# Performance work log

Hardware: AMD Instinct MI355X
Metric: run time of the kernel (lower is better)

## Reference

```python
import jax, jax.numpy as jnp
import numpy as np

B, S, D, H = 4, 2048, 1024, 16
DH = D // H


def setup_inputs() -> dict:
    key = jax.random.key(0)
    ks = jax.random.split(key, 11)
    s = 1.0 / np.sqrt(D)
    return {
        "q": jax.random.normal(ks[0], (B, S, D), jnp.float32),
        "k": jax.random.normal(ks[1], (B, S, D), jnp.float32),
        "v": jax.random.normal(ks[2], (B, S, D), jnp.float32),
        "Wq": jax.random.normal(ks[3], (D, D), jnp.float32) * s,
        "bq": jnp.zeros((D,), jnp.float32),
        "Wk": jax.random.normal(ks[4], (D, D), jnp.float32) * s,
        "bk": jnp.zeros((D,), jnp.float32),
        "Wv": jax.random.normal(ks[5], (D, D), jnp.float32) * s,
        "bv": jnp.zeros((D,), jnp.float32),
        "Wo": jax.random.normal(ks[6], (D, D), jnp.float32) * s,
        "bo": jnp.zeros((D,), jnp.float32),
    }


def _split_heads(x):
    # (B, S, D) -> (B, H, S, DH)
    b, s, _ = x.shape
    return x.reshape(b, s, H, DH).transpose(0, 2, 1, 3)


def reference(q, k, v, Wq, bq, Wk, bk, Wv, bv, Wo, bo):
    # torch Linear: x @ W.T + b
    qh = _split_heads(q @ Wq.T + bq)
    kh = _split_heads(k @ Wk.T + bk)
    vh = _split_heads(v @ Wv.T + bv)
    scale = 1.0 / jnp.sqrt(jnp.asarray(DH, qh.dtype))
    scores = jnp.einsum("bhqd,bhkd->bhqk", qh, kh) * scale  # (B,H,S,S)
    probs = jax.nn.softmax(scores, axis=-1)
    ctx = jnp.einsum("bhqk,bhkd->bhqd", probs, vh)  # (B,H,S,DH)
    x = ctx.transpose(0, 2, 1, 3).reshape(q.shape[0], -1, D)
    return x @ Wo.T + bo
```

## Files before the change

kernel.cpp:

```cpp
#include <hip/hip_runtime.h>

typedef __bf16 bf16x8 __attribute__((ext_vector_type(8)));
typedef __bf16 bf16x4 __attribute__((ext_vector_type(4)));
typedef _Float16 f16x8 __attribute__((ext_vector_type(8)));
typedef _Float16 f16x4v __attribute__((ext_vector_type(4)));
typedef __fp16 fp16x2 __attribute__((ext_vector_type(2)));
typedef float f32x4 __attribute__((ext_vector_type(4)));
typedef float f32x16 __attribute__((ext_vector_type(16)));
typedef unsigned short u16;
typedef unsigned int u32;
typedef unsigned int u32x4 __attribute__((ext_vector_type(4)));

constexpr int Bc = 4, Sc = 2048, Dc = 1024, Hc = 16, DHc = 64;
constexpr int Mrows = Bc * Sc;
constexpr size_t MK = (size_t)Mrows * Dc;
constexpr size_t WK = (size_t)Dc * Dc;

__device__ __forceinline__ u16 f2bf(float f) {
  u32 u = __float_as_uint(f);
  u = (u + 0x7fffu + ((u >> 16) & 1u)) >> 16;
  return (u16)u;
}

#define LDSP(p) ((__attribute__((address_space(3))) void*)(p))
#define GLBP(p) ((const __attribute__((address_space(1))) void*)(p))

__global__ __launch_bounds__(256) void cvt4_kernel(const float* __restrict__ a,
                                                   const float* __restrict__ b,
                                                   const float* __restrict__ c,
                                                   const float* __restrict__ d,
                                                   ushort4* __restrict__ out, int n4) {
  const float4* in = (const float4*)(blockIdx.y == 0 ? a : blockIdx.y == 1 ? b
                                     : blockIdx.y == 2 ? c : d);
  ushort4* o = out + (size_t)blockIdx.y * n4;
  int stride = gridDim.x * blockDim.x;
  for (int i = blockIdx.x * blockDim.x + threadIdx.x; i < n4; i += stride) {
    float4 v = in[i];
    ushort4 r;
    r.x = f2bf(v.x); r.y = f2bf(v.y); r.z = f2bf(v.z); r.w = f2bf(v.w);
    o[i] = r;
  }
}

__global__ __launch_bounds__(256, 2) void gemmqkv(const float* __restrict__ Aq,
                                                  const float* __restrict__ Ak,
                                                  const float* __restrict__ Av,
                                                  const u16* __restrict__ Bt0,
                                                  const float* __restrict__ b0,
                                                  const float* __restrict__ b1,
                                                  const float* __restrict__ b2,
                                                  void* __restrict__ out0) {
  constexpr int K = 1024, NT = 32;
  __shared__ u16 lds[3 * 12288];

  const int y = blockIdx.y;
  const float* A = (y == 0) ? Aq : (y == 1) ? Ak : Av;
  const u16* Bt = Bt0 + (size_t)y * WK;
  const float* bias = (y == 0) ? b0 : (y == 1) ? b1 : b2;

  const int wg = (blockIdx.x & 7) * 32 + (blockIdx.x >> 3);
  const int tm = wg >> 3, tn = wg & 7;
  const int row0 = tm << 8, col0 = tn << 7;

  const int t_ = threadIdx.x, w = t_ >> 6, l = t_ & 63;
  const int wm = w >> 1, wn = w & 1;
  const int col = l & 31, hh = l >> 5;

  f32x16 acc[4][2] = {};
  float4 areg[8];

  auto ldA = [&](int tile) {
#pragma unroll
    for (int i = 0; i < 4; ++i) {
      const int r = (w * 4 + i) * 16 + (l >> 2);
      const float* p = A + (size_t)(row0 + r) * K + (tile << 5) + (l & 3) * 8;
      areg[2 * i] = *(const float4*)p;
      areg[2 * i + 1] = *(const float4*)(p + 4);
    }
  };
  auto wrA = [&](int tile) {
    u16* buf = &lds[(tile % 3) * 12288];
#pragma unroll
    for (int i = 0; i < 4; ++i) {
      const int r = (w * 4 + i) * 16 + (l >> 2);
      u32 d0, d1, d2, d3;
      asm("v_cvt_pk_bf16_f32 %0, %1, %2" : "=v"(d0) : "v"(areg[2 * i].x), "v"(areg[2 * i].y));
      asm("v_cvt_pk_bf16_f32 %0, %1, %2" : "=v"(d1) : "v"(areg[2 * i].z), "v"(areg[2 * i].w));
      asm("v_cvt_pk_bf16_f32 %0, %1, %2" : "=v"(d2) : "v"(areg[2 * i + 1].x), "v"(areg[2 * i + 1].y));
      asm("v_cvt_pk_bf16_f32 %0, %1, %2" : "=v"(d3) : "v"(areg[2 * i + 1].z), "v"(areg[2 * i + 1].w));
      u32x4 pk; pk[0] = d0; pk[1] = d1; pk[2] = d2; pk[3] = d3;
      const int g = (l & 3) ^ ((r >> 1) & 3);
      *(u32x4*)((char*)buf + r * 64 + g * 16) = pk;
    }
  };
  auto stB = [&](int tile, int i) {
    u16* buf = &lds[(tile % 3) * 12288] + 8192;
    const int c = w * 2 + i;
    const int r = c * 16 + (l >> 2);
    const int sg = (l & 3) ^ ((r >> 1) & 3);
    __builtin_amdgcn_global_load_lds(
        GLBP(Bt + (size_t)(col0 + r) * K + (tile << 5) + sg * 8),
        LDSP(buf + c * 512), 16, 0, 0);
  };

  ldA(0);
  stB(0, 0); stB(0, 1);
  stB(1, 0); stB(1, 1);
  asm volatile("s_waitcnt vmcnt(2)" ::: "memory");
  wrA(0);
  ldA(1);
  asm volatile("s_waitcnt lgkmcnt(0)" ::: "memory");
  __builtin_amdgcn_s_barrier();

#pragma unroll 1
  for (int t = 0; t < NT; ++t) {
    const u16* abuf = &lds[(t % 3) * 12288];
    const u16* bbuf = abuf + 8192;
    if (t + 2 < NT) { stB(t + 2, 0); stB(t + 2, 1); }
    bf16x8 af[2][4], bf[2][2];
#pragma unroll
    for (int kc = 0; kc < 2; ++kc) {
      const int g = kc * 2 + hh;
#pragma unroll
      for (int mb = 0; mb < 4; ++mb) {
        const int ar = wm * 128 + mb * 32 + col;
        af[kc][mb] = *(const bf16x8*)&abuf[ar * 32 + ((g ^ ((ar >> 1) & 3)) << 3)];
      }
#pragma unroll
      for (int nb = 0; nb < 2; ++nb) {
        const int br = wn * 64 + nb * 32 + col;
        bf[kc][nb] = *(const bf16x8*)&bbuf[br * 32 + ((g ^ ((br >> 1) & 3)) << 3)];
      }
    }
    __builtin_amdgcn_s_setprio(1);
#pragma unroll
    for (int kc = 0; kc < 2; ++kc)
#pragma unroll
      for (int mb = 0; mb < 4; ++mb)
#pragma unroll
        for (int nb = 0; nb < 2; ++nb)
          acc[mb][nb] = __builtin_amdgcn_mfma_f32_32x32x16_bf16(af[kc][mb], bf[kc][nb],
                                                               acc[mb][nb], 0, 0, 0);
    __builtin_amdgcn_s_setprio(0);
    if (t + 1 < NT) {
      if (t + 2 < NT) asm volatile("s_waitcnt vmcnt(2)" ::: "memory");
      else            asm volatile("s_waitcnt vmcnt(0)" ::: "memory");
      wrA(t + 1);
      if (t + 2 < NT) ldA(t + 2);
    }
    asm volatile("s_waitcnt lgkmcnt(0)" ::: "memory");
    __builtin_amdgcn_s_barrier();
  }

#pragma unroll
  for (int mb = 0; mb < 4; ++mb)
#pragma unroll
    for (int nb = 0; nb < 2; ++nb) {
      const int n = col0 + wn * 64 + nb * 32 + col;
      const float bv = bias[n];
      const int mbase = row0 + wm * 128 + mb * 32 + 4 * hh;
      if (y == 2) {
        u16* Vt = (u16*)out0 + 2 * MK;
        const int h = n >> 6, dh = n & 63;
#pragma unroll
        for (int qg = 0; qg < 4; ++qg) {
          const int s0 = mbase + 8 * qg;
          const int b = s0 >> 11, s = s0 & (Sc - 1);
          f16x4v pk;
#pragma unroll
          for (int r4 = 0; r4 < 4; ++r4) pk[r4] = (_Float16)(acc[mb][nb][qg * 4 + r4] + bv);
          *(f16x4v*)&Vt[((size_t)((b * Hc + h) * DHc + dh)) * Sc + s] = pk;
        }
      } else {
        u16* Oh = (u16*)out0 + (size_t)y * MK;
        const float scl = (y == 0) ? 0.125f * 1.44269504089f : 1.f;
        const int h = n >> 6, dh = n & 63;
#pragma unroll
        for (int r = 0; r < 16; ++r) {
          const int m = mbase + (r & 3) + 8 * (r >> 2);
          const int b = m >> 11, s = m & (Sc - 1);
          Oh[((size_t)((b * Hc + h) * Sc + s)) * DHc + dh] = f2bf((acc[mb][nb][r] + bv) * scl);
        }
      }
    }
}

__global__ __launch_bounds__(256, 2) void gemmout(const u16* __restrict__ A,
                                                  const u16* __restrict__ Bt,
                                                  const float* __restrict__ bias,
                                                  float* __restrict__ O) {
  constexpr int K = 1024, NT = 32;
  __shared__ u16 lds[3 * 12288];

  const int wg = (blockIdx.x & 7) * 32 + (blockIdx.x >> 3);
  const int tm = wg >> 3, tn = wg & 7;
  const int row0 = tm << 8, col0 = tn << 7;

  const int t_ = threadIdx.x, w = t_ >> 6, l = t_ & 63;
  const int wm = w >> 1, wn = w & 1;
  const int col = l & 31, hh = l >> 5;

  f32x16 acc[4][2] = {};

  auto stA = [&](int tile, int i) {
    u16* buf = &lds[(tile % 3) * 12288];
    const int c = w * 4 + i;
    const int r = c * 16 + (l >> 2);
    const int sg = (l & 3) ^ ((r >> 1) & 3);
    __builtin_amdgcn_global_load_lds(
        GLBP(A + (size_t)(row0 + r) * K + (tile << 5) + sg * 8),
        LDSP(buf + c * 512), 16, 0, 0);
  };
  auto stB = [&](int tile, int i) {
    u16* buf = &lds[(tile % 3) * 12288] + 8192;
    const int c = w * 2 + i;
    const int r = c * 16 + (l >> 2);
    const int sg = (l & 3) ^ ((r >> 1) & 3);
    __builtin_amdgcn_global_load_lds(
        GLBP(Bt + (size_t)(col0 + r) * K + (tile << 5) + sg * 8),
        LDSP(buf + c * 512), 16, 0, 0);
  };

  stA(0, 0); stA(0, 1); stA(0, 2); stA(0, 3); stB(0, 0); stB(0, 1);
  stA(1, 0); stA(1, 1); stA(1, 2); stA(1, 3); stB(1, 0); stB(1, 1);
  asm volatile("s_waitcnt vmcnt(6)" ::: "memory");
  __builtin_amdgcn_s_barrier();

#pragma unroll 1
  for (int t = 0; t < NT; ++t) {
    const u16* abuf = &lds[(t % 3) * 12288];
    const u16* bbuf = abuf + 8192;
    if (t + 2 < NT) {
      stA(t + 2, 0); stA(t + 2, 1); stA(t + 2, 2); stA(t + 2, 3);
      stB(t + 2, 0); stB(t + 2, 1);
    }
    bf16x8 af[2][4], bf[2][2];
#pragma unroll
    for (int kc = 0; kc < 2; ++kc) {
      const int g = kc * 2 + hh;
#pragma unroll
      for (int mb = 0; mb < 4; ++mb) {
        const int ar = wm * 128 + mb * 32 + col;
        af[kc][mb] = *(const bf16x8*)&abuf[ar * 32 + ((g ^ ((ar >> 1) & 3)) << 3)];
      }
#pragma unroll
      for (int nb = 0; nb < 2; ++nb) {
        const int br = wn * 64 + nb * 32 + col;
        bf[kc][nb] = *(const bf16x8*)&bbuf[br * 32 + ((g ^ ((br >> 1) & 3)) << 3)];
      }
    }
    __builtin_amdgcn_s_setprio(1);
#pragma unroll
    for (int kc = 0; kc < 2; ++kc)
#pragma unroll
      for (int mb = 0; mb < 4; ++mb)
#pragma unroll
        for (int nb = 0; nb < 2; ++nb)
          acc[mb][nb] = __builtin_amdgcn_mfma_f32_32x32x16_bf16(af[kc][mb], bf[kc][nb],
                                                               acc[mb][nb], 0, 0, 0);
    __builtin_amdgcn_s_setprio(0);
    if (t + 2 < NT)      asm volatile("s_waitcnt vmcnt(6)" ::: "memory");
    else if (t + 1 < NT) asm volatile("s_waitcnt vmcnt(0)" ::: "memory");
    __builtin_amdgcn_s_barrier();
  }

#pragma unroll
  for (int mb = 0; mb < 4; ++mb)
#pragma unroll
    for (int nb = 0; nb < 2; ++nb) {
      const int n = col0 + wn * 64 + nb * 32 + col;
      const float bv = bias[n];
      const int mbase = row0 + wm * 128 + mb * 32 + 4 * hh;
#pragma unroll
      for (int r = 0; r < 16; ++r) {
        const int m = mbase + (r & 3) + 8 * (r >> 2);
        O[(size_t)m * Dc + n] = acc[mb][nb][r] + bv;
      }
    }
}

__global__ __launch_bounds__(256, 4) void attn5_kernel(const u16* __restrict__ Qh,
                                                       const u16* __restrict__ Kh,
                                                       const u16* __restrict__ Vt,
                                                       u16* __restrict__ ctx) {
  __shared__ u16 smem[16384];
  u16* K_lds = smem;
  u16* V_lds = smem + 8192;

  const int wid = (blockIdx.x & 7) * 128 + (blockIdx.x >> 3);
  const int qt = wid & 15, bh = wid >> 4;
  const int t = threadIdx.x, w = t >> 6, l = t & 63;
  const int q = l & 31, h = l >> 5;
  const int q0 = qt * 128 + w * 32;

  bf16x8 qf[4];
  {
    const u16* qp = Qh + ((size_t)bh * Sc + q0 + q) * DHc + h * 8;
#pragma unroll
    for (int kk = 0; kk < 4; ++kk) qf[kk] = *(const bf16x8*)(qp + kk * 16);
  }

  f32x16 oacc[2] = {};
  float l_run = 0.f;
  const fp16x2 ones2 = {(__fp16)1.f, (__fp16)1.f};

  const int lrow = l >> 3, lg = l & 7;

  auto stage = [&](int tile, int buf) {
    const int kt = tile << 6;
    u16* Kb = K_lds + buf * 4096;
    u16* Vb = V_lds + buf * 4096;
#pragma unroll
    for (int c = 0; c < 2; ++c) {
      const int rb = w * 16 + c * 8;
      const int row = rb + lrow;
      const int sg = lg ^ (row & 7);
      __builtin_amdgcn_global_load_lds(GLBP(Kh + ((size_t)bh * Sc + kt + row) * DHc + sg * 8),
                                       LDSP(&Kb[rb * 64]), 16, 0, 0);
      __builtin_amdgcn_global_load_lds(GLBP(Vt + ((size_t)bh * DHc + row) * Sc + kt + sg * 8),
                                       LDSP(&Vb[rb * 64]), 16, 0, 0);
    }
  };

  stage(0, 0);
  __syncthreads();

#pragma unroll 1
  for (int tile = 0; tile < 32; ++tile) {
    const int cur = tile & 1;
    if (tile + 1 < 32) stage(tile + 1, cur ^ 1);
    const u16* Kb = K_lds + cur * 4096;
    const u16* Vb = V_lds + cur * 4096;

    f32x16 sacc[2] = {};
    __builtin_amdgcn_s_setprio(1);
#pragma unroll
    for (int kk = 0; kk < 4; ++kk) {
      const int kr0 = q, kr1 = 32 + q;
      bf16x8 kf0 = *(const bf16x8*)&Kb[kr0 * 64 + ((2 * kk + h) ^ (kr0 & 7)) * 8];
      bf16x8 kf1 = *(const bf16x8*)&Kb[kr1 * 64 + ((2 * kk + h) ^ (kr1 & 7)) * 8];
      sacc[0] = __builtin_amdgcn_mfma_f32_32x32x16_bf16(kf0, qf[kk], sacc[0], 0, 0, 0);
      sacc[1] = __builtin_amdgcn_mfma_f32_32x32x16_bf16(kf1, qf[kk], sacc[1], 0, 0, 0);
    }
    __builtin_amdgcn_s_setprio(0);

    float sumA = 0.f, sumB = 0.f;
#pragma unroll
    for (int kt32 = 0; kt32 < 2; ++kt32)
#pragma unroll
      for (int c = 0; c < 2; ++c) {
        float p0 = __builtin_amdgcn_exp2f(sacc[kt32][c * 8 + 0]);
        float p1 = __builtin_amdgcn_exp2f(sacc[kt32][c * 8 + 1]);
        float p2 = __builtin_amdgcn_exp2f(sacc[kt32][c * 8 + 2]);
        float p3 = __builtin_amdgcn_exp2f(sacc[kt32][c * 8 + 3]);
        float p4 = __builtin_amdgcn_exp2f(sacc[kt32][c * 8 + 4]);
        float p5 = __builtin_amdgcn_exp2f(sacc[kt32][c * 8 + 5]);
        float p6 = __builtin_amdgcn_exp2f(sacc[kt32][c * 8 + 6]);
        float p7 = __builtin_amdgcn_exp2f(sacc[kt32][c * 8 + 7]);
        fp16x2 X0 = __builtin_amdgcn_cvt_pkrtz(p0, p1);
        fp16x2 X1 = __builtin_amdgcn_cvt_pkrtz(p2, p3);
        fp16x2 Y0 = __builtin_amdgcn_cvt_pkrtz(p4, p5);
        fp16x2 Y1 = __builtin_amdgcn_cvt_pkrtz(p6, p7);
        sumA = __builtin_amdgcn_fdot2(X0, ones2, sumA, false);
        sumA = __builtin_amdgcn_fdot2(X1, ones2, sumA, false);
        sumB = __builtin_amdgcn_fdot2(Y0, ones2, sumB, false);
        sumB = __builtin_amdgcn_fdot2(Y1, ones2, sumB, false);
        auto rA = __builtin_amdgcn_permlane32_swap(__builtin_bit_cast(u32, X0),
                                                   __builtin_bit_cast(u32, Y0), false, false);
        auto rB = __builtin_amdgcn_permlane32_swap(__builtin_bit_cast(u32, X1),
                                                   __builtin_bit_cast(u32, Y1), false, false);
        u32x4 wv;
        wv[0] = rA[0]; wv[1] = rB[0]; wv[2] = rA[1]; wv[3] = rB[1];
        f16x8 pf = __builtin_bit_cast(f16x8, wv);
        const int gb = kt32 * 4 + c * 2 + h;
        __builtin_amdgcn_s_setprio(1);
#pragma unroll
        for (int dt = 0; dt < 2; ++dt) {
          const int vrow = dt * 32 + q;
          f16x8 vf = *(const f16x8*)&Vb[vrow * 64 + ((gb ^ (vrow & 7)) * 8)];
          oacc[dt] = __builtin_amdgcn_mfma_f32_32x32x16_f16(vf, pf, oacc[dt], 0, 0, 0);
        }
        __builtin_amdgcn_s_setprio(0);
      }
    l_run += sumA + sumB;
    __syncthreads();
  }

  l_run += __shfl_xor(l_run, 32);
  const float inv = 1.f / l_run;
  u16* E = smem + w * 2048;
#pragma unroll
  for (int dt = 0; dt < 2; ++dt)
#pragma unroll
    for (int rg = 0; rg < 4; ++rg) {
      bf16x4 pk;
#pragma unroll
      for (int j = 0; j < 4; ++j) pk[j] = (__bf16)(oacc[dt][rg * 4 + j] * inv);
      const int dh0 = dt * 32 + rg * 8 + 4 * h;
      int byte = q * 128 + dh0 * 2;
      byte ^= (q & 7) << 4;
      *(bf16x4*)((char*)E + byte) = pk;
    }
  __syncthreads();
  const int b = bh >> 4, head = bh & 15;
  const size_t crow = ((size_t)(b * Sc + q0 + q)) * Dc + head * 64 + h * 32;
#pragma unroll
  for (int i = 0; i < 4; ++i) {
    const int g = (4 * h + i) ^ (q & 7);
    uint4 tv = *(const uint4*)((char*)E + q * 128 + g * 16);
    *(uint4*)((u16*)ctx + crow + i * 8) = tv;
  }
}

extern "C" void kernel_launch(void* const* d_in, const int* in_sizes, int n_in,
                              void* d_out, int out_size, void* d_ws, size_t ws_size,
                              hipStream_t stream) {
  const float* q  = (const float*)d_in[0];
  const float* k  = (const float*)d_in[1];
  const float* v  = (const float*)d_in[2];
  const float* Wq = (const float*)d_in[3];
  const float* bq = (const float*)d_in[4];
  const float* Wk = (const float*)d_in[5];
  const float* bk = (const float*)d_in[6];
  const float* Wv = (const float*)d_in[7];
  const float* bv = (const float*)d_in[8];
  const float* Wo = (const float*)d_in[9];
  const float* bo = (const float*)d_in[10];
  float* out = (float*)d_out;

  u16* Wqb = (u16*)d_ws;
  u16* Qh  = Wqb + 4 * WK;
  u16* Kh  = Qh + MK;
  u16* VtB = Kh + MK;
  u16* ctx = VtB + MK;

  cvt4_kernel<<<dim3(512, 4), 256, 0, stream>>>(Wq, Wk, Wv, Wo, (ushort4*)Wqb, (int)(WK / 4));

  gemmqkv<<<dim3(256, 3), 256, 0, stream>>>(q, k, v, Wqb, bq, bk, bv, (void*)Qh);

  attn5_kernel<<<1024, 256, 0, stream>>>(Qh, Kh, VtB, ctx);

  gemmout<<<256, 256, 0, stream>>>(ctx, Wqb + 3 * WK, bo, out);
}
```

Baseline: 200.2 us.

## Double-buffer A register prefetch in QKV projection GEMM main loop

Uses two register buffers for the fp32 A tiles, so the global load for tile t+2 is issued at the start of iteration t rather than after the MFMA block. The loop is unrolled by two to ping-pong between the buffers, and the vmcnt waits are adjusted to match. The per-kc fragment loads are also interleaved with their MFMAs, which lowers the number of live fragment registers. The aim is to hide global A-load latency behind compute, at the cost of more VGPRs for the second A buffer and fragile hand-tuned waitcnt values.

```diff
diff --git a/kernel.cpp b/kernel.cpp
--- a/kernel.cpp
+++ b/kernel.cpp
@@ -67,27 +67,27 @@
   const int col = l & 31, hh = l >> 5;
 
   f32x16 acc[4][2] = {};
-  float4 areg[8];
-
-  auto ldA = [&](int tile) {
+  float4 aregA[8], aregB[8];
+
+  auto ldA = [&](int tile, float4* dst) {
 #pragma unroll
     for (int i = 0; i < 4; ++i) {
       const int r = (w * 4 + i) * 16 + (l >> 2);
       const float* p = A + (size_t)(row0 + r) * K + (tile << 5) + (l & 3) * 8;
-      areg[2 * i] = *(const float4*)p;
-      areg[2 * i + 1] = *(const float4*)(p + 4);
-    }
-  };
-  auto wrA = [&](int tile) {
+      dst[2 * i] = *(const float4*)p;
+      dst[2 * i + 1] = *(const float4*)(p + 4);
+    }
+  };
+  auto wrA = [&](int tile, const float4* src) {
     u16* buf = &lds[(tile % 3) * 12288];
 #pragma unroll
     for (int i = 0; i < 4; ++i) {
       const int r = (w * 4 + i) * 16 + (l >> 2);
       u32 d0, d1, d2, d3;
-      asm("v_cvt_pk_bf16_f32 %0, %1, %2" : "=v"(d0) : "v"(areg[2 * i].x), "v"(areg[2 * i].y));
-      asm("v_cvt_pk_bf16_f32 %0, %1, %2" : "=v"(d1) : "v"(areg[2 * i].z), "v"(areg[2 * i].w));
-      asm("v_cvt_pk_bf16_f32 %0, %1, %2" : "=v"(d2) : "v"(areg[2 * i + 1].x), "v"(areg[2 * i + 1].y));
-      asm("v_cvt_pk_bf16_f32 %0, %1, %2" : "=v"(d3) : "v"(areg[2 * i + 1].z), "v"(areg[2 * i + 1].w));
+      asm("v_cvt_pk_bf16_f32 %0, %1, %2" : "=v"(d0) : "v"(src[2 * i].x), "v"(src[2 * i].y));
+      asm("v_cvt_pk_bf16_f32 %0, %1, %2" : "=v"(d1) : "v"(src[2 * i].z), "v"(src[2 * i].w));
+      asm("v_cvt_pk_bf16_f32 %0, %1, %2" : "=v"(d2) : "v"(src[2 * i + 1].x), "v"(src[2 * i + 1].y));
+      asm("v_cvt_pk_bf16_f32 %0, %1, %2" : "=v"(d3) : "v"(src[2 * i + 1].z), "v"(src[2 * i + 1].w));
       u32x4 pk; pk[0] = d0; pk[1] = d1; pk[2] = d2; pk[3] = d3;
       const int g = (l & 3) ^ ((r >> 1) & 3);
       *(u32x4*)((char*)buf + r * 64 + g * 16) = pk;
@@ -103,53 +103,59 @@
         LDSP(buf + c * 512), 16, 0, 0);
   };
 
-  ldA(0);
+  ldA(0, aregA);
   stB(0, 0); stB(0, 1);
   stB(1, 0); stB(1, 1);
-  asm volatile("s_waitcnt vmcnt(2)" ::: "memory");
-  wrA(0);
-  ldA(1);
+  asm volatile("s_waitcnt vmcnt(4)" ::: "memory");
+  wrA(0, aregA);
+  ldA(1, aregB);
+  asm volatile("s_waitcnt vmcnt(10)" ::: "memory");
   asm volatile("s_waitcnt lgkmcnt(0)" ::: "memory");
   __builtin_amdgcn_s_barrier();
 
-#pragma unroll 1
-  for (int t = 0; t < NT; ++t) {
+  auto tile_body = [&](int t, float4* ldst, const float4* wsrc) {
     const u16* abuf = &lds[(t % 3) * 12288];
     const u16* bbuf = abuf + 8192;
-    if (t + 2 < NT) { stB(t + 2, 0); stB(t + 2, 1); }
-    bf16x8 af[2][4], bf[2][2];
+    if (t + 2 < NT) {
+      stB(t + 2, 0); stB(t + 2, 1);
+      ldA(t + 2, ldst);
+    }
 #pragma unroll
     for (int kc = 0; kc < 2; ++kc) {
       const int g = kc * 2 + hh;
+      bf16x8 af[4], bf[2];
 #pragma unroll
       for (int mb = 0; mb < 4; ++mb) {
         const int ar = wm * 128 + mb * 32 + col;
-        af[kc][mb] = *(const bf16x8*)&abuf[ar * 32 + ((g ^ ((ar >> 1) & 3)) << 3)];
+        af[mb] = *(const bf16x8*)&abuf[ar * 32 + ((g ^ ((ar >> 1) & 3)) << 3)];
       }
 #pragma unroll
       for (int nb = 0; nb < 2; ++nb) {
         const int br = wn * 64 + nb * 32 + col;
-        bf[kc][nb] = *(const bf16x8*)&bbuf[br * 32 + ((g ^ ((br >> 1) & 3)) << 3)];
-      }
-    }
-    __builtin_amdgcn_s_setprio(1);
-#pragma unroll
-    for (int kc = 0; kc < 2; ++kc)
+        bf[nb] = *(const bf16x8*)&bbuf[br * 32 + ((g ^ ((br >> 1) & 3)) << 3)];
+      }
+      __builtin_amdgcn_s_setprio(1);
 #pragma unroll
       for (int mb = 0; mb < 4; ++mb)
 #pragma unroll
         for (int nb = 0; nb < 2; ++nb)
-          acc[mb][nb] = __builtin_amdgcn_mfma_f32_32x32x16_bf16(af[kc][mb], bf[kc][nb],
+          acc[mb][nb] = __builtin_amdgcn_mfma_f32_32x32x16_bf16(af[mb], bf[nb],
                                                                acc[mb][nb], 0, 0, 0);
-    __builtin_amdgcn_s_setprio(0);
+      __builtin_amdgcn_s_setprio(0);
+    }
+    if (t + 2 < NT)      asm volatile("s_waitcnt vmcnt(10)" ::: "memory");
+    else if (t + 1 < NT) asm volatile("s_waitcnt vmcnt(0)" ::: "memory");
     if (t + 1 < NT) {
-      if (t + 2 < NT) asm volatile("s_waitcnt vmcnt(2)" ::: "memory");
-      else            asm volatile("s_waitcnt vmcnt(0)" ::: "memory");
-      wrA(t + 1);
-      if (t + 2 < NT) ldA(t + 2);
-    }
-    asm volatile("s_waitcnt lgkmcnt(0)" ::: "memory");
+      wrA(t + 1, wsrc);
+      asm volatile("s_waitcnt lgkmcnt(0)" ::: "memory");
+    }
     __builtin_amdgcn_s_barrier();
+  };
+
+#pragma unroll 1
+  for (int t = 0; t < NT; t += 2) {
+    tile_body(t, aregA, aregB);
+    tile_body(t + 1, aregB, aregA);
   }
 
 #pragma unroll
```

Result: no change. 200.7 us (+0.2%).

## Stream fp32 A tiles directly to LDS and convert to bf16 at fragment load

Applied to the files above, without the earlier changes.

The QKV projection GEMM stops loading fp32 A into registers, converting to bf16 and writing to LDS. It now uses global_load_lds to copy fp32 A tiles straight into a double-buffered, XOR-swizzled LDS area and converts to bf16 when reading MFMA fragments. This removes register staging and the explicit LDS writes, and the B pipeline drops from triple to double buffering with prefetch distance one. In exchange the A tile takes twice the LDS bytes, every wave repeats the conversion on each fragment read, and waiting vmcnt(0) each iteration may expose global load latency.

```diff
diff --git a/kernel.cpp b/kernel.cpp
--- a/kernel.cpp
+++ b/kernel.cpp
@@ -51,7 +51,7 @@
                                                   const float* __restrict__ b2,
                                                   void* __restrict__ out0) {
   constexpr int K = 1024, NT = 32;
-  __shared__ u16 lds[3 * 12288];
+  __shared__ u32x4 smem[5120];
 
   const int y = blockIdx.y;
   const float* A = (y == 0) ? Aq : (y == 1) ? Ak : Av;
@@ -67,34 +67,21 @@
   const int col = l & 31, hh = l >> 5;
 
   f32x16 acc[4][2] = {};
-  float4 areg[8];
-
-  auto ldA = [&](int tile) {
-#pragma unroll
-    for (int i = 0; i < 4; ++i) {
-      const int r = (w * 4 + i) * 16 + (l >> 2);
-      const float* p = A + (size_t)(row0 + r) * K + (tile << 5) + (l & 3) * 8;
-      areg[2 * i] = *(const float4*)p;
-      areg[2 * i + 1] = *(const float4*)(p + 4);
-    }
-  };
-  auto wrA = [&](int tile) {
-    u16* buf = &lds[(tile % 3) * 12288];
-#pragma unroll
-    for (int i = 0; i < 4; ++i) {
-      const int r = (w * 4 + i) * 16 + (l >> 2);
-      u32 d0, d1, d2, d3;
-      asm("v_cvt_pk_bf16_f32 %0, %1, %2" : "=v"(d0) : "v"(areg[2 * i].x), "v"(areg[2 * i].y));
-      asm("v_cvt_pk_bf16_f32 %0, %1, %2" : "=v"(d1) : "v"(areg[2 * i].z), "v"(areg[2 * i].w));
-      asm("v_cvt_pk_bf16_f32 %0, %1, %2" : "=v"(d2) : "v"(areg[2 * i + 1].x), "v"(areg[2 * i + 1].y));
-      asm("v_cvt_pk_bf16_f32 %0, %1, %2" : "=v"(d3) : "v"(areg[2 * i + 1].z), "v"(areg[2 * i + 1].w));
-      u32x4 pk; pk[0] = d0; pk[1] = d1; pk[2] = d2; pk[3] = d3;
-      const int g = (l & 3) ^ ((r >> 1) & 3);
-      *(u32x4*)((char*)buf + r * 64 + g * 16) = pk;
+
+  auto stA = [&](int tile) {
+    float* buf = (float*)smem + (tile & 1) * 8192;
+#pragma unroll
+    for (int i = 0; i < 8; ++i) {
+      const int c = w * 8 + i;
+      const int r = c * 8 + (l >> 3);
+      const int sg = (l & 7) ^ (r & 7);
+      __builtin_amdgcn_global_load_lds(
+          GLBP(A + (size_t)(row0 + r) * K + (tile << 5) + sg * 4),
+          LDSP(buf + c * 256), 16, 0, 0);
     }
   };
   auto stB = [&](int tile, int i) {
-    u16* buf = &lds[(tile % 3) * 12288] + 8192;
+    u16* buf = (u16*)smem + 32768 + (tile & 1) * 4096;
     const int c = w * 2 + i;
     const int r = c * 16 + (l >> 2);
     const int sg = (l & 3) ^ ((r >> 1) & 3);
@@ -103,29 +90,34 @@
         LDSP(buf + c * 512), 16, 0, 0);
   };
 
-  ldA(0);
-  stB(0, 0); stB(0, 1);
-  stB(1, 0); stB(1, 1);
-  asm volatile("s_waitcnt vmcnt(2)" ::: "memory");
-  wrA(0);
-  ldA(1);
-  asm volatile("s_waitcnt lgkmcnt(0)" ::: "memory");
+  stA(0); stB(0, 0); stB(0, 1);
+  asm volatile("s_waitcnt vmcnt(0)" ::: "memory");
   __builtin_amdgcn_s_barrier();
 
 #pragma unroll 1
   for (int t = 0; t < NT; ++t) {
-    const u16* abuf = &lds[(t % 3) * 12288];
-    const u16* bbuf = abuf + 8192;
-    if (t + 2 < NT) { stB(t + 2, 0); stB(t + 2, 1); }
+    const float* abuf = (const float*)smem + (t & 1) * 8192;
+    const u16* bbuf = (const u16*)smem + 32768 + (t & 1) * 4096;
+    if (t + 1 < NT) { stA(t + 1); stB(t + 1, 0); stB(t + 1, 1); }
+
     bf16x8 af[2][4], bf[2][2];
 #pragma unroll
     for (int kc = 0; kc < 2; ++kc) {
-      const int g = kc * 2 + hh;
+      const int J = 2 * (2 * kc + hh);
 #pragma unroll
       for (int mb = 0; mb < 4; ++mb) {
         const int ar = wm * 128 + mb * 32 + col;
-        af[kc][mb] = *(const bf16x8*)&abuf[ar * 32 + ((g ^ ((ar >> 1) & 3)) << 3)];
-      }
+        f32x4 lo = *(const f32x4*)&abuf[ar * 32 + ((J ^ (ar & 7)) << 2)];
+        f32x4 hi = *(const f32x4*)&abuf[ar * 32 + (((J + 1) ^ (ar & 7)) << 2)];
+        u32 d0, d1, d2, d3;
+        asm("v_cvt_pk_bf16_f32 %0, %1, %2" : "=v"(d0) : "v"(lo[0]), "v"(lo[1]));
+        asm("v_cvt_pk_bf16_f32 %0, %1, %2" : "=v"(d1) : "v"(lo[2]), "v"(lo[3]));
+        asm("v_cvt_pk_bf16_f32 %0, %1, %2" : "=v"(d2) : "v"(hi[0]), "v"(hi[1]));
+        asm("v_cvt_pk_bf16_f32 %0, %1, %2" : "=v"(d3) : "v"(hi[2]), "v"(hi[3]));
+        u32x4 pk; pk[0] = d0; pk[1] = d1; pk[2] = d2; pk[3] = d3;
+        af[kc][mb] = __builtin_bit_cast(bf16x8, pk);
+      }
+      const int g = kc * 2 + hh;
 #pragma unroll
       for (int nb = 0; nb < 2; ++nb) {
         const int br = wn * 64 + nb * 32 + col;
@@ -142,13 +134,7 @@
           acc[mb][nb] = __builtin_amdgcn_mfma_f32_32x32x16_bf16(af[kc][mb], bf[kc][nb],
                                                                acc[mb][nb], 0, 0, 0);
     __builtin_amdgcn_s_setprio(0);
-    if (t + 1 < NT) {
-      if (t + 2 < NT) asm volatile("s_waitcnt vmcnt(2)" ::: "memory");
-      else            asm volatile("s_waitcnt vmcnt(0)" ::: "memory");
-      wrA(t + 1);
-      if (t + 2 < NT) ldA(t + 2);
-    }
-    asm volatile("s_waitcnt lgkmcnt(0)" ::: "memory");
+    if (t + 1 < NT) asm volatile("s_waitcnt vmcnt(0)" ::: "memory");
     __builtin_amdgcn_s_barrier();
   }
 
```

New measurement: 211.8 us. 5.8% more time.

## Software-pipeline attention with triple-buffered K/V and overlapped QK and softmax-PV

Applied to the files above, without the earlier changes.

The attention kernel moves from double to triple buffering of K/V tiles in LDS and restructures the loop so the QK MFMA of the next tile is issued before the softmax/PV of the current tile, using two ping-ponged score accumulators. This is meant to hide LDS load latency and overlap the exp/convert work with matrix ops. In exchange it uses more LDS and registers, and launch bounds drop from 4 to 3 blocks per CU, which lowers occupancy. A separate vmcnt wait is also added in the GEMM prologue.

```diff
diff --git a/kernel.cpp b/kernel.cpp
--- a/kernel.cpp
+++ b/kernel.cpp
@@ -109,6 +109,7 @@
   asm volatile("s_waitcnt vmcnt(2)" ::: "memory");
   wrA(0);
   ldA(1);
+  asm volatile("s_waitcnt vmcnt(10)" ::: "memory");
   asm volatile("s_waitcnt lgkmcnt(0)" ::: "memory");
   __builtin_amdgcn_s_barrier();
 
@@ -279,13 +280,13 @@
     }
 }
 
-__global__ __launch_bounds__(256, 4) void attn5_kernel(const u16* __restrict__ Qh,
+__global__ __launch_bounds__(256, 3) void attn6_kernel(const u16* __restrict__ Qh,
                                                        const u16* __restrict__ Kh,
                                                        const u16* __restrict__ Vt,
                                                        u16* __restrict__ ctx) {
-  __shared__ u16 smem[16384];
+  __shared__ u16 smem[24576];
   u16* K_lds = smem;
-  u16* V_lds = smem + 8192;
+  u16* V_lds = smem + 12288;
 
   const int wid = (blockIdx.x & 7) * 128 + (blockIdx.x >> 3);
   const int qt = wid & 15, bh = wid >> 4;
@@ -306,10 +307,10 @@
 
   const int lrow = l >> 3, lg = l & 7;
 
-  auto stage = [&](int tile, int buf) {
+  auto stage = [&](int tile) {
     const int kt = tile << 6;
-    u16* Kb = K_lds + buf * 4096;
-    u16* Vb = V_lds + buf * 4096;
+    u16* Kb = K_lds + (tile % 3) * 4096;
+    u16* Vb = V_lds + (tile % 3) * 4096;
 #pragma unroll
     for (int c = 0; c < 2; ++c) {
       const int rb = w * 16 + c * 8;
@@ -322,17 +323,10 @@
     }
   };
 
-  stage(0, 0);
-  __syncthreads();
-
-#pragma unroll 1
-  for (int tile = 0; tile < 32; ++tile) {
-    const int cur = tile & 1;
-    if (tile + 1 < 32) stage(tile + 1, cur ^ 1);
-    const u16* Kb = K_lds + cur * 4096;
-    const u16* Vb = V_lds + cur * 4096;
-
-    f32x16 sacc[2] = {};
+  auto qk = [&](int tile, f32x16* sacc) {
+    const u16* Kb = K_lds + (tile % 3) * 4096;
+    sacc[0] = (f32x16){};
+    sacc[1] = (f32x16){};
     __builtin_amdgcn_s_setprio(1);
 #pragma unroll
     for (int kk = 0; kk < 4; ++kk) {
@@ -343,7 +337,10 @@
       sacc[1] = __builtin_amdgcn_mfma_f32_32x32x16_bf16(kf1, qf[kk], sacc[1], 0, 0, 0);
     }
     __builtin_amdgcn_s_setprio(0);
-
+  };
+
+  auto smpv = [&](int tile, const f32x16* sacc) {
+    const u16* Vb = V_lds + (tile % 3) * 4096;
     float sumA = 0.f, sumB = 0.f;
 #pragma unroll
     for (int kt32 = 0; kt32 < 2; ++kt32)
@@ -383,9 +380,28 @@
         __builtin_amdgcn_s_setprio(0);
       }
     l_run += sumA + sumB;
+  };
+
+  f32x16 saccA[2], saccB[2];
+
+  stage(0);
+  __syncthreads();
+  stage(1);
+  qk(0, saccA);
+
+#pragma unroll 1
+  for (int i = 0; i < 32; i += 2) {
     __syncthreads();
-  }
-
+    if (i + 2 < 32) stage(i + 2);
+    if (i + 1 < 32) qk(i + 1, saccB);
+    smpv(i, saccA);
+    __syncthreads();
+    if (i + 3 < 32) stage(i + 3);
+    if (i + 2 < 32) qk(i + 2, saccA);
+    if (i + 1 < 32) smpv(i + 1, saccB);
+  }
+
+  __syncthreads();
   l_run += __shfl_xor(l_run, 32);
   const float inv = 1.f / l_run;
   u16* E = smem + w * 2048;
@@ -438,7 +454,7 @@
 
   gemmqkv<<<dim3(256, 3), 256, 0, stream>>>(q, k, v, Wqb, bq, bk, bv, (void*)Qh);
 
-  attn5_kernel<<<1024, 256, 0, stream>>>(Qh, Kh, VtB, ctx);
+  attn6_kernel<<<1024, 256, 0, stream>>>(Qh, Kh, VtB, ctx);
 
   gemmout<<<256, 256, 0, stream>>>(ctx, Wqb + 3 * WK, bo, out);
 }
```

Measured after the change: 207.9 us. 1.04x slower.
